# Kernel optimization log

Measured on AMD Instinct MI355X. Metric: run time of the kernel, lower is better.

The kernel has to match this reference:

```python
import jax, jax.numpy as jnp
import numpy as np

N_HEADS = 16

def setup_inputs() -> dict:
    key = jax.random.key(0)
    k1, k2, k3 = jax.random.split(key, 3)
    B, T, C = 4, 2048, 1024
    x = jax.random.normal(k1, (B, T, C), dtype=jnp.float32)
    w_qkv = jax.random.normal(k2, (C, 3 * C), dtype=jnp.float32) * (1.0 / np.sqrt(C))
    w_out = jax.random.normal(k3, (C, C), dtype=jnp.float32) * (1.0 / np.sqrt(C))
    return {"x": x, "w_qkv": w_qkv, "w_out": w_out}

def reference(x, w_qkv, w_out):
    B, T, C = x.shape
    H = N_HEADS
    d_k = C // H
    qkv = x @ w_qkv                       # (B,T,3C)
    q, k, v = jnp.split(qkv, 3, axis=-1)
    # (B,H,T,d_k)
    q = q.reshape(B, T, H, d_k).transpose(0, 2, 1, 3)
    k = k.reshape(B, T, H, d_k).transpose(0, 2, 1, 3)
    v = v.reshape(B, T, H, d_k).transpose(0, 2, 1, 3)
    scale = 1.0 / np.sqrt(d_k)
    scores = jnp.einsum('bhqd,bhkd->bhqk', q, k) * scale  # (B,H,T,T)
    causal = jnp.triu(jnp.ones((T, T), dtype=bool), k=1)  # True = ignore
    scores = jnp.where(causal, -jnp.inf, scores)
    weights = jax.nn.softmax(scores, axis=-1)
    out = jnp.einsum('bhqk,bhkd->bhqd', weights, v)       # (B,H,T,d_k)
    out = out.transpose(0, 2, 1, 3).reshape(B, T, C)
    return out @ w_out
```

## Files before the change

### kernel.cpp

```cpp
#include <hip/hip_runtime.h>
#include <hip/hip_bf16.h>
#include <stdint.h>
#include <math.h>

typedef __bf16 bf16;
typedef __bf16 bf16x4 __attribute__((ext_vector_type(4)));
typedef __bf16 bf16x8 __attribute__((ext_vector_type(8)));
typedef float f32x4 __attribute__((ext_vector_type(4)));

#define BB 4
#define TT 2048
#define CC 1024
#define HH 16
#define DK 64

__device__ __forceinline__ void gl_lds16(const void* gsrc, void* ldst) {
    __builtin_amdgcn_global_load_lds(
        (__attribute__((address_space(1))) void*)(void*)(gsrc),
        (__attribute__((address_space(3))) void*)(ldst),
        16, 0, 0);
}

__device__ __forceinline__ void bar() {
    asm volatile("" ::: "memory");
    __builtin_amdgcn_s_barrier();
    asm volatile("" ::: "memory");
}
#define VMCNT(N) asm volatile("s_waitcnt vmcnt(" #N ")" ::: "memory")

__global__ __launch_bounds__(256) void prep(
    const float* __restrict__ x, const float* __restrict__ wq,
    const float* __restrict__ wo, bf16* __restrict__ xbf,
    bf16* __restrict__ wqT, bf16* __restrict__ woT) {
    __shared__ bf16 tile[32][33];
    const int bid = blockIdx.x, tid = threadIdx.x;
    if (bid < 4096) {
        const int i = (bid * 256 + tid) * 8;
        const f32x4 a = *(const f32x4*)(x + i);
        const f32x4 b = *(const f32x4*)(x + i + 4);
        bf16x8 o;
#pragma unroll
        for (int j = 0; j < 4; ++j) { o[j] = (bf16)a[j]; o[j + 4] = (bf16)b[j]; }
        *(bf16x8*)(xbf + i) = o;
        return;
    }
    const float* in;
    bf16* out;
    int R, C, c0, r0;
    if (bid < 7168) {
        const int tb = bid - 4096;
        in = wq; out = wqT; R = 1024; C = 3072;
        c0 = (tb % 96) * 32; r0 = (tb / 96) * 32;
    } else {
        const int tb = bid - 7168;
        in = wo; out = woT; R = 1024; C = 1024;
        c0 = (tb % 32) * 32; r0 = (tb / 32) * 32;
    }
    const int tx = tid & 31, ty = tid >> 5;
#pragma unroll
    for (int i = 0; i < 32; i += 8)
        tile[ty + i][tx] = (bf16)in[(size_t)(r0 + ty + i) * C + c0 + tx];
    __syncthreads();
#pragma unroll
    for (int i = 0; i < 32; i += 8)
        out[(size_t)(c0 + ty + i) * R + r0 + tx] = tile[tx][ty + i];
}

template <int EPI>
__global__ __launch_bounds__(512, 2) void gemm256(
    const bf16* __restrict__ A, const bf16* __restrict__ Bt,
    void* __restrict__ Cq, bf16* __restrict__ Kh, bf16* __restrict__ Vt,
    int M, int N, int K) {
    __shared__ bf16 As[2][256 * 64];
    __shared__ bf16 Bs[2][256 * 64];
    const int tid = threadIdx.x;
    const int w = tid >> 6, l = tid & 63;
    const int wm = w >> 2, wn = w & 3;
    const int lm = l & 15, lq = l >> 4;
    const int m0 = blockIdx.y * 256, n0 = blockIdx.x * 256;

    const int srow_a = w * 8 + (l >> 3);
    const int srow_b = (w & 3) * 8 + (w >> 2) * 64 + (l >> 3);
    const int csw = ((l & 7) ^ (l >> 3)) * 8;
    const bf16* agl = A + (size_t)(m0 + srow_a) * K + csw;
    const bf16* bgl = Bt + (size_t)(n0 + srow_b) * K + csw;
    const int wa = w * 8;
    const int wb = (w & 3) * 8 + (w >> 2) * 64;

    int aoff[2], boff[2];
#pragma unroll
    for (int ks = 0; ks < 2; ++ks) {
        const int sl = (ks * 4 + lq) ^ (lm & 7);
        aoff[ks] = (wm * 128 + lm) * 64 + sl * 8;
        boff[ks] = (wn * 64 + lm) * 64 + sl * 8;
    }

    f32x4 acc[8][4] = {};
    bf16x8 af[4][2], bfA[2][2], bfB[2][2];

#define STGA(R, DSTA, KOFF) gl_lds16(agl + (size_t)(R) * K + (KOFF), (DSTA) + (wa + (R)) * 64)
#define STGB(R, DSTB, KOFF) gl_lds16(bgl + (size_t)(R) * K + (KOFF), (DSTB) + (wb + (R)) * 64)
#define LDA(MIH, SRC)                                                          \
    _Pragma("unroll") for (int mi = 0; mi < 4; ++mi)                           \
    _Pragma("unroll") for (int ks = 0; ks < 2; ++ks)                           \
        af[mi][ks] = *(const bf16x8*)((SRC) + aoff[ks] + ((MIH) * 4 + mi) * 1024);
#define LDB(BF, NIH, SRC)                                                      \
    _Pragma("unroll") for (int ni = 0; ni < 2; ++ni)                           \
    _Pragma("unroll") for (int ks = 0; ks < 2; ++ks)                           \
        BF[ni][ks] = *(const bf16x8*)((SRC) + boff[ks] + ((NIH) * 2 + ni) * 1024);
#define QMFMA(MIH, NIH, BF)                                                    \
    __builtin_amdgcn_s_setprio(1);                                             \
    _Pragma("unroll") for (int ks = 0; ks < 2; ++ks)                           \
    _Pragma("unroll") for (int mi = 0; mi < 4; ++mi)                           \
    _Pragma("unroll") for (int ni = 0; ni < 2; ++ni)                           \
        acc[(MIH) * 4 + mi][(NIH) * 2 + ni] =                                  \
            __builtin_amdgcn_mfma_f32_16x16x32_bf16(                           \
                af[mi][ks], BF[ni][ks], acc[(MIH) * 4 + mi][(NIH) * 2 + ni],   \
                0, 0, 0);                                                      \
    __builtin_amdgcn_s_setprio(0);

    bf16* A0 = &As[0][0]; bf16* A1 = &As[1][0];
    bf16* B0 = &Bs[0][0]; bf16* B1 = &Bs[1][0];
    const int NT = K >> 6;

    STGA(0, A0, 0); STGA(128, A0, 0);
    STGB(0, B0, 0); STGB(128, B0, 0);
    STGB(32, B0, 0); STGB(160, B0, 0);
    STGA(64, A0, 0); STGA(192, A0, 0);
    VMCNT(4); bar();

    for (int t = 0; t < NT - 1; ++t) {
        const int bb = t & 1;
        const bf16* Ac = bb ? A1 : A0; const bf16* Bc = bb ? B1 : B0;
        bf16* An = bb ? A0 : A1;       bf16* Bn = bb ? B0 : B1;
        const int k1 = (t + 1) << 6;
        LDA(0, Ac); LDB(bfA, 0, Bc);
        STGA(0, An, k1); STGA(128, An, k1);
        bar();
        QMFMA(0, 0, bfA);
        VMCNT(4); bar();
        LDB(bfB, 1, Bc);
        STGB(0, Bn, k1); STGB(128, Bn, k1);
        bar();
        QMFMA(0, 1, bfB);
        VMCNT(4); bar();
        LDA(1, Ac);
        STGB(32, Bn, k1); STGB(160, Bn, k1);
        bar();
        QMFMA(1, 1, bfB);
        bar();
        STGA(64, An, k1); STGA(192, An, k1);
        bar();
        QMFMA(1, 0, bfA);
        VMCNT(4); bar();
    }
    {
        const int bb = (NT - 1) & 1;
        const bf16* Ac = bb ? A1 : A0; const bf16* Bc = bb ? B1 : B0;
        LDA(0, Ac); LDB(bfA, 0, Bc);
        bar(); QMFMA(0, 0, bfA); VMCNT(2); bar();
        LDB(bfB, 1, Bc);
        bar(); QMFMA(0, 1, bfB); VMCNT(0); bar();
        LDA(1, Ac);
        bar(); QMFMA(1, 1, bfB); bar();
        QMFMA(1, 0, bfA);
    }

    if (EPI == 0) {
#pragma unroll
        for (int mi = 0; mi < 8; ++mi) {
            const int row = m0 + wm * 128 + mi * 16 + lq * 4;
#pragma unroll
            for (int ni = 0; ni < 4; ++ni) {
                const int col = n0 + wn * 64 + ni * 16 + lm;
#pragma unroll
                for (int r = 0; r < 4; ++r)
                    ((float*)Cq)[(size_t)(row + r) * N + col] = acc[mi][ni][r];
            }
        }
    } else {
        bf16* Q = (bf16*)Cq;
#pragma unroll
        for (int ni = 0; ni < 4; ++ni) {
            const int c = n0 + wn * 64 + ni * 16 + lm;
            const int part = c >> 10;
            const int h = (c & 1023) >> 6;
            const int d = c & 63;
#pragma unroll
            for (int mi = 0; mi < 8; ++mi) {
                const int rowg = m0 + wm * 128 + mi * 16 + lq * 4;
#pragma unroll
                for (int r = 0; r < 4; ++r) {
                    const int rg = rowg + r;
                    const int b = rg >> 11, t = rg & 2047;
                    const bf16 v = (bf16)acc[mi][ni][r];
                    if (part == 0)
                        Q[((size_t)(b * HH + h) * TT + t) * DK + d] = v;
                    else if (part == 1)
                        Kh[((size_t)(b * HH + h) * TT + t) * DK + d] = v;
                    else
                        Vt[((size_t)(b * HH + h) * DK + d) * TT + t] = v;
                }
            }
        }
    }
#undef STGA
#undef STGB
#undef LDA
#undef LDB
#undef QMFMA
}

template <int EPI>
__global__ __launch_bounds__(256) void gemm_bt(
    const bf16* __restrict__ A, const bf16* __restrict__ Bt,
    void* __restrict__ Cq, bf16* __restrict__ Kh, bf16* __restrict__ Vt,
    int M, int N, int K) {
    __shared__ bf16 As[128 * 32];
    __shared__ bf16 Bs[128 * 32];
    const int tid = threadIdx.x;
    const int w = tid >> 6, l = tid & 63;
    const int wm = w >> 1, wn = w & 1;
    const int m0 = blockIdx.y * 128, n0 = blockIdx.x * 128;
    const int lr4 = l >> 2, lc4 = (l & 3) * 8;
    const int lm = l & 15, lq = l >> 4;

    f32x4 acc[4][4] = {};

    for (int k0 = 0; k0 < K; k0 += 32) {
#pragma unroll
        for (int i = 0; i < 2; ++i) {
            const int j = w * 2 + i;
            gl_lds16(A + (size_t)(m0 + j * 16 + lr4) * K + k0 + lc4, As + j * 512);
            gl_lds16(Bt + (size_t)(n0 + j * 16 + lr4) * K + k0 + lc4, Bs + j * 512);
        }
        __syncthreads();
        bf16x8 af[4], bfr[4];
#pragma unroll
        for (int mi = 0; mi < 4; ++mi)
            af[mi] = *(const bf16x8*)(As + (wm * 64 + mi * 16 + lm) * 32 + lq * 8);
#pragma unroll
        for (int ni = 0; ni < 4; ++ni)
            bfr[ni] = *(const bf16x8*)(Bs + (wn * 64 + ni * 16 + lm) * 32 + lq * 8);
#pragma unroll
        for (int mi = 0; mi < 4; ++mi)
#pragma unroll
            for (int ni = 0; ni < 4; ++ni)
                acc[mi][ni] = __builtin_amdgcn_mfma_f32_16x16x32_bf16(
                    af[mi], bfr[ni], acc[mi][ni], 0, 0, 0);
        __syncthreads();
    }

    if (EPI == 0) {
#pragma unroll
        for (int mi = 0; mi < 4; ++mi) {
            const int row = m0 + wm * 64 + mi * 16 + lq * 4;
#pragma unroll
            for (int ni = 0; ni < 4; ++ni) {
                const int col = n0 + wn * 64 + ni * 16 + lm;
#pragma unroll
                for (int r = 0; r < 4; ++r)
                    ((float*)Cq)[(size_t)(row + r) * N + col] = acc[mi][ni][r];
            }
        }
    } else {
        bf16* Q = (bf16*)Cq;
#pragma unroll
        for (int ni = 0; ni < 4; ++ni) {
            const int c = n0 + wn * 64 + ni * 16 + lm;
            const int part = c >> 10;
            const int h = (c & 1023) >> 6;
            const int d = c & 63;
#pragma unroll
            for (int mi = 0; mi < 4; ++mi) {
                const int rowg = m0 + wm * 64 + mi * 16 + lq * 4;
#pragma unroll
                for (int r = 0; r < 4; ++r) {
                    const int rg = rowg + r;
                    const int b = rg >> 11, t = rg & 2047;
                    const bf16 v = (bf16)acc[mi][ni][r];
                    if (part == 0)
                        Q[((size_t)(b * HH + h) * TT + t) * DK + d] = v;
                    else if (part == 1)
                        Kh[((size_t)(b * HH + h) * TT + t) * DK + d] = v;
                    else
                        Vt[((size_t)(b * HH + h) * DK + d) * TT + t] = v;
                }
            }
        }
    }
}

#define PAD 72
__global__ __launch_bounds__(256, 4) void attn_kernel(
    const bf16* __restrict__ Qh, const bf16* __restrict__ Kh,
    const bf16* __restrict__ Vt, bf16* __restrict__ O) {
    __shared__ bf16 Ks[2][64 * PAD];
    __shared__ bf16 Vs[2][64 * PAD];
    const int tid = threadIdx.x, w = tid >> 6, l = tid & 63;
    const int lm = l & 15, lq = l >> 4;
    const int id = blockIdx.x;
    const int xcd = id & 7;
    const int rest = id >> 3;
    const int bh = xcd + 8 * (rest >> 4);
    const int p = rest & 15;
    const int b = bh >> 4, h = bh & 15;
    const bf16* Qb = Qh + (size_t)bh * TT * DK;
    const bf16* Kb = Kh + (size_t)bh * TT * DK;
    const bf16* Vb = Vt + (size_t)bh * DK * TT;
    const int srow = tid >> 3, scol = (tid & 7) * 8;
    const int prow = w * 8 + (lm & 7) + ((lm >> 3) << 5);

    const float smul = 0.125f * 1.44269504088896340736f;
    const int qts[2] = {p, 31 - p};

    bf16x8 kreg[2], vreg[2];
#pragma unroll
    for (int i = 0; i < 2; ++i) {
        kreg[i] = *(const bf16x8*)(Kb + (size_t)(srow + i * 32) * DK + scol);
        vreg[i] = *(const bf16x8*)(Vb + (size_t)(srow + i * 32) * TT + scol);
    }
    int buf = 0;

#pragma unroll
    for (int half = 0; half < 2; ++half) {
        const int qt = qts[half];
        const int q0 = qt * 64;
        const int qg = q0 + w * 16 + lm;

        bf16x8 qf[2];
#pragma unroll
        for (int ks = 0; ks < 2; ++ks)
            qf[ks] = *(const bf16x8*)(Qb + (size_t)(q0 + w * 16 + lm) * DK +
                                      ks * 32 + lq * 8);

        f32x4 oacc[4] = {};
        float lrun = 0.f;

        for (int kt = 0; kt <= qt; ++kt) {
#pragma unroll
            for (int i = 0; i < 2; ++i) {
                *(bf16x8*)(Ks[buf] + (srow + i * 32) * PAD + scol) = kreg[i];
                *(bf16x8*)(Vs[buf] + (srow + i * 32) * PAD + scol) = vreg[i];
            }
            __syncthreads();

            bf16* Pp = Ks[buf ^ 1];

            {
                int nkt = -1;
                if (kt < qt) nkt = kt + 1;
                else if (half == 0) nkt = 0;
                if (nkt >= 0) {
#pragma unroll
                    for (int i = 0; i < 2; ++i) {
                        kreg[i] = *(const bf16x8*)(
                            Kb + (size_t)(nkt * 64 + srow + i * 32) * DK + scol);
                        vreg[i] = *(const bf16x8*)(
                            Vb + (size_t)(srow + i * 32) * TT + nkt * 64 + scol);
                    }
                }
            }

            f32x4 st[4] = {};
            __builtin_amdgcn_s_setprio(1);
#pragma unroll
            for (int ks = 0; ks < 2; ++ks) {
#pragma unroll
                for (int nb = 0; nb < 4; ++nb) {
                    const bf16x8 kf = *(const bf16x8*)(Ks[buf] + (nb * 16 + lm) * PAD +
                                                       ks * 32 + lq * 8);
                    st[nb] = __builtin_amdgcn_mfma_f32_16x16x32_bf16(
                        kf, qf[ks], st[nb], 0, 0, 0);
                }
            }
            __builtin_amdgcn_s_setprio(0);

            const bool diag = (kt == qt);
#pragma unroll
            for (int nb = 0; nb < 4; ++nb) {
                bf16x4 pk;
#pragma unroll
                for (int r = 0; r < 4; ++r) {
                    float arg = fmaf(st[nb][r], smul, -20.f);
                    if (diag) {
                        const int keyg = kt * 64 + nb * 16 + lq * 4 + r;
                        if (keyg > qg) arg = -1e30f;
                    }
                    const float pv = exp2f(arg);
                    lrun += pv;
                    pk[r] = (bf16)pv;
                }
                *(bf16x4*)(Pp + prow * PAD + nb * 16 + lq * 4) = pk;
            }

            __builtin_amdgcn_s_setprio(1);
#pragma unroll
            for (int ks = 0; ks < 2; ++ks) {
                const bf16x8 pf =
                    *(const bf16x8*)(Pp + prow * PAD + ks * 32 + lq * 8);
#pragma unroll
                for (int ni = 0; ni < 4; ++ni) {
                    const bf16x8 vf = *(const bf16x8*)(Vs[buf] + (ni * 16 + lm) * PAD +
                                                       ks * 32 + lq * 8);
                    oacc[ni] = __builtin_amdgcn_mfma_f32_16x16x32_bf16(
                        pf, vf, oacc[ni], 0, 0, 0);
                }
            }
            __builtin_amdgcn_s_setprio(0);
            buf ^= 1;
        }

        lrun += __shfl_xor(lrun, 16);
        lrun += __shfl_xor(lrun, 32);
        float linv[4];
#pragma unroll
        for (int r = 0; r < 4; ++r) linv[r] = 1.0f / __shfl(lrun, lq * 4 + r);
#pragma unroll
        for (int ni = 0; ni < 4; ++ni) {
            const int col = h * 64 + ni * 16 + lm;
#pragma unroll
            for (int r = 0; r < 4; ++r) {
                const int t = q0 + w * 16 + lq * 4 + r;
                O[((size_t)(b * TT + t)) * CC + col] = (bf16)(oacc[ni][r] * linv[r]);
            }
        }
    }
}

extern "C" void kernel_launch(void* const* d_in, const int* in_sizes, int n_in,
                              void* d_out, int out_size, void* d_ws, size_t ws_size,
                              hipStream_t stream) {
    const float* x = (const float*)d_in[0];
    const float* w_qkv = (const float*)d_in[1];
    const float* w_out = (const float*)d_in[2];

    char* ws = (char*)d_ws;
    const size_t M1 = (size_t)1 << 20;
    bf16* Qh = (bf16*)(ws);
    bf16* Kh = (bf16*)(ws + 16 * M1);
    bf16* Vt = (bf16*)(ws + 32 * M1);
    bf16* Ob = (bf16*)(ws + 48 * M1);
    bf16* wqkvT = (bf16*)(ws + 64 * M1);
    bf16* woutT = (bf16*)(ws + 70 * M1);
    bf16* xbf = (bf16*)(ws + 72 * M1);

    prep<<<8192, 256, 0, stream>>>(x, w_qkv, w_out, xbf, wqkvT, woutT);
    gemm256<1><<<dim3(3072 / 256, 8192 / 256), 512, 0, stream>>>(
        xbf, wqkvT, Qh, Kh, Vt, 8192, 3072, 1024);
    attn_kernel<<<1024, 256, 0, stream>>>(Qh, Kh, Vt, Ob);
    gemm_bt<0><<<dim3(1024 / 128, 8192 / 128), 256, 0, stream>>>(
        Ob, woutT, (float*)d_out, nullptr, nullptr, 8192, 1024, 1024);
}
```

Before: 274.3 us.

## Split attention block into two wave groups sharing K/V tiles for adjacent query tiles

The attention kernel grows from 256 to 512 threads. Each block now processes two adjacent query tiles at once, one per group of four waves, and both groups share a single K/V staging stream per block. This replaces the old scheme where one block walked a short and a long query tile one after the other. The aim is to halve K/V global loads per query tile and shorten each block's serial critical path. In exchange, work per block is now uneven (from 2 up to 32 KV iterations), one group sits idle on the last iteration, and LDS per block grows by an extra P buffer. The launch bound of 512 threads with 4 blocks per CU may also squeeze the register budget.

```diff
diff --git a/kernel.cpp b/kernel.cpp
--- a/kernel.cpp
+++ b/kernel.cpp
@@ -292,84 +292,66 @@
 }
 
 #define PAD 72
-__global__ __launch_bounds__(256, 4) void attn_kernel(
+__global__ __launch_bounds__(512, 4) void attn_kernel(
     const bf16* __restrict__ Qh, const bf16* __restrict__ Kh,
     const bf16* __restrict__ Vt, bf16* __restrict__ O) {
     __shared__ bf16 Ks[2][64 * PAD];
     __shared__ bf16 Vs[2][64 * PAD];
+    __shared__ bf16 Ps[2][64 * PAD];
     const int tid = threadIdx.x, w = tid >> 6, l = tid & 63;
+    const int wq2 = w >> 2, wl = w & 3;
     const int lm = l & 15, lq = l >> 4;
     const int id = blockIdx.x;
     const int xcd = id & 7;
     const int rest = id >> 3;
     const int bh = xcd + 8 * (rest >> 4);
-    const int p = rest & 15;
+    const int pp = rest & 15;
+    const int pi = (pp & 1) ? (15 - (pp >> 1)) : (pp >> 1);
     const int b = bh >> 4, h = bh & 15;
+    const int NT = 2 * pi + 2;
+    const int qt = 2 * pi + 1 - wq2;
+    const int myNT = NT - wq2;
     const bf16* Qb = Qh + (size_t)bh * TT * DK;
     const bf16* Kb = Kh + (size_t)bh * TT * DK;
     const bf16* Vb = Vt + (size_t)bh * DK * TT;
     const int srow = tid >> 3, scol = (tid & 7) * 8;
-    const int prow = w * 8 + (lm & 7) + ((lm >> 3) << 5);
 
     const float smul = 0.125f * 1.44269504088896340736f;
-    const int qts[2] = {p, 31 - p};
-
-    bf16x8 kreg[2], vreg[2];
-#pragma unroll
-    for (int i = 0; i < 2; ++i) {
-        kreg[i] = *(const bf16x8*)(Kb + (size_t)(srow + i * 32) * DK + scol);
-        vreg[i] = *(const bf16x8*)(Vb + (size_t)(srow + i * 32) * TT + scol);
-    }
+
+    bf16x8 kreg = *(const bf16x8*)(Kb + (size_t)srow * DK + scol);
+    bf16x8 vreg = *(const bf16x8*)(Vb + (size_t)srow * TT + scol);
+
+    const int q0 = qt * 64;
+    const int qg = q0 + wl * 16 + lm;
+    bf16x8 qf[2];
+#pragma unroll
+    for (int ks = 0; ks < 2; ++ks)
+        qf[ks] = *(const bf16x8*)(Qb + (size_t)qg * DK + ks * 32 + lq * 8);
+
+    bf16* Pb = Ps[wq2];
+    f32x4 oacc[4] = {};
+    float lrun = 0.f;
     int buf = 0;
 
-#pragma unroll
-    for (int half = 0; half < 2; ++half) {
-        const int qt = qts[half];
-        const int q0 = qt * 64;
-        const int qg = q0 + w * 16 + lm;
-
-        bf16x8 qf[2];
-#pragma unroll
-        for (int ks = 0; ks < 2; ++ks)
-            qf[ks] = *(const bf16x8*)(Qb + (size_t)(q0 + w * 16 + lm) * DK +
-                                      ks * 32 + lq * 8);
-
-        f32x4 oacc[4] = {};
-        float lrun = 0.f;
-
-        for (int kt = 0; kt <= qt; ++kt) {
-#pragma unroll
-            for (int i = 0; i < 2; ++i) {
-                *(bf16x8*)(Ks[buf] + (srow + i * 32) * PAD + scol) = kreg[i];
-                *(bf16x8*)(Vs[buf] + (srow + i * 32) * PAD + scol) = vreg[i];
-            }
-            __syncthreads();
-
-            bf16* Pp = Ks[buf ^ 1];
-
-            {
-                int nkt = -1;
-                if (kt < qt) nkt = kt + 1;
-                else if (half == 0) nkt = 0;
-                if (nkt >= 0) {
-#pragma unroll
-                    for (int i = 0; i < 2; ++i) {
-                        kreg[i] = *(const bf16x8*)(
-                            Kb + (size_t)(nkt * 64 + srow + i * 32) * DK + scol);
-                        vreg[i] = *(const bf16x8*)(
-                            Vb + (size_t)(srow + i * 32) * TT + nkt * 64 + scol);
-                    }
-                }
-            }
-
+    for (int kt = 0; kt < NT; ++kt) {
+        *(bf16x8*)(Ks[buf] + srow * PAD + scol) = kreg;
+        *(bf16x8*)(Vs[buf] + srow * PAD + scol) = vreg;
+        __syncthreads();
+
+        if (kt + 1 < NT) {
+            kreg = *(const bf16x8*)(Kb + (size_t)((kt + 1) * 64 + srow) * DK + scol);
+            vreg = *(const bf16x8*)(Vb + (size_t)srow * TT + (kt + 1) * 64 + scol);
+        }
+
+        if (kt < myNT) {
             f32x4 st[4] = {};
             __builtin_amdgcn_s_setprio(1);
 #pragma unroll
             for (int ks = 0; ks < 2; ++ks) {
 #pragma unroll
                 for (int nb = 0; nb < 4; ++nb) {
-                    const bf16x8 kf = *(const bf16x8*)(Ks[buf] + (nb * 16 + lm) * PAD +
-                                                       ks * 32 + lq * 8);
+                    const bf16x8 kf = *(const bf16x8*)(
+                        Ks[buf] + (nb * 16 + lm) * PAD + ks * 32 + lq * 8);
                     st[nb] = __builtin_amdgcn_mfma_f32_16x16x32_bf16(
                         kf, qf[ks], st[nb], 0, 0, 0);
                 }
@@ -391,39 +373,39 @@
                     lrun += pv;
                     pk[r] = (bf16)pv;
                 }
-                *(bf16x4*)(Pp + prow * PAD + nb * 16 + lq * 4) = pk;
+                *(bf16x4*)(Pb + (wl * 16 + lm) * PAD + nb * 16 + lq * 4) = pk;
             }
 
             __builtin_amdgcn_s_setprio(1);
 #pragma unroll
             for (int ks = 0; ks < 2; ++ks) {
                 const bf16x8 pf =
-                    *(const bf16x8*)(Pp + prow * PAD + ks * 32 + lq * 8);
+                    *(const bf16x8*)(Pb + (wl * 16 + lm) * PAD + ks * 32 + lq * 8);
 #pragma unroll
                 for (int ni = 0; ni < 4; ++ni) {
-                    const bf16x8 vf = *(const bf16x8*)(Vs[buf] + (ni * 16 + lm) * PAD +
-                                                       ks * 32 + lq * 8);
+                    const bf16x8 vf = *(const bf16x8*)(
+                        Vs[buf] + (ni * 16 + lm) * PAD + ks * 32 + lq * 8);
                     oacc[ni] = __builtin_amdgcn_mfma_f32_16x16x32_bf16(
                         pf, vf, oacc[ni], 0, 0, 0);
                 }
             }
             __builtin_amdgcn_s_setprio(0);
-            buf ^= 1;
-        }
-
-        lrun += __shfl_xor(lrun, 16);
-        lrun += __shfl_xor(lrun, 32);
-        float linv[4];
-#pragma unroll
-        for (int r = 0; r < 4; ++r) linv[r] = 1.0f / __shfl(lrun, lq * 4 + r);
-#pragma unroll
-        for (int ni = 0; ni < 4; ++ni) {
-            const int col = h * 64 + ni * 16 + lm;
-#pragma unroll
-            for (int r = 0; r < 4; ++r) {
-                const int t = q0 + w * 16 + lq * 4 + r;
-                O[((size_t)(b * TT + t)) * CC + col] = (bf16)(oacc[ni][r] * linv[r]);
-            }
+        }
+        buf ^= 1;
+    }
+
+    lrun += __shfl_xor(lrun, 16);
+    lrun += __shfl_xor(lrun, 32);
+    float linv[4];
+#pragma unroll
+    for (int r = 0; r < 4; ++r) linv[r] = 1.0f / __shfl(lrun, lq * 4 + r);
+#pragma unroll
+    for (int ni = 0; ni < 4; ++ni) {
+        const int col = h * 64 + ni * 16 + lm;
+#pragma unroll
+        for (int r = 0; r < 4; ++r) {
+            const int t = q0 + wl * 16 + lq * 4 + r;
+            O[((size_t)(b * TT + t)) * CC + col] = (bf16)(oacc[ni][r] * linv[r]);
         }
     }
 }
@@ -448,7 +430,7 @@
     prep<<<8192, 256, 0, stream>>>(x, w_qkv, w_out, xbf, wqkvT, woutT);
     gemm256<1><<<dim3(3072 / 256, 8192 / 256), 512, 0, stream>>>(
         xbf, wqkvT, Qh, Kh, Vt, 8192, 3072, 1024);
-    attn_kernel<<<1024, 256, 0, stream>>>(Qh, Kh, Vt, Ob);
+    attn_kernel<<<1024, 512, 0, stream>>>(Qh, Kh, Vt, Ob);
     gemm_bt<0><<<dim3(1024 / 128, 8192 / 128), 256, 0, stream>>>(
         Ob, woutT, (float*)d_out, nullptr, nullptr, 8192, 1024, 1024);
 }
```

After: 326.8 us. 19.2% more time.
